# Performance work log

Measured on AMD Instinct MI355X. Metric: run time of the kernel, lower is better.

Reference implementation:

```python
import jax, jax.numpy as jnp
import numpy as np

# cfg constants (init_kwargs)
NMS_THRESH = 0.6
CONF_THRESH = 0.05
TOPN = 1000           # nms_thresh_topN: pre-NMS cap and post-NMS cap
NUM_CLASSES = 80
CLS_OFFSET = 4096.0   # > max image coord; class-aware NMS via coordinate offset


def setup_inputs() -> dict:
    key = jax.random.key(0)
    k0, k1, k2, k3 = jax.random.split(key, 4)
    B, H, W, C = 16, 128, 128, NUM_CLASSES
    N = H * W
    image_h, image_w = 1024, 1024
    # anchor-point pixel coordinates for this FPN level
    locations = jax.random.uniform(k0, (N, 2), dtype=jnp.float32) * 1024.0
    pred_cls = jax.random.normal(k1, (B, H, W, C), dtype=jnp.float32)
    # (l, t, r, b) distances are positive
    pred_boxes = jax.random.uniform(k2, (B, H, W, 4), dtype=jnp.float32) * 64.0
    pred_centerness = jax.random.normal(k3, (B, H, W), dtype=jnp.float32)
    return {"locations": locations, "pred_cls": pred_cls, "pred_boxes": pred_boxes,
            "pred_centerness": pred_centerness, "image_h": image_h, "image_w": image_w}


def _pairwise_iou(b):  # b: [K, 4] xyxy
    x1, y1, x2, y2 = b[:, 0], b[:, 1], b[:, 2], b[:, 3]
    area = jnp.maximum(x2 - x1, 0.0) * jnp.maximum(y2 - y1, 0.0)
    ix1 = jnp.maximum(x1[:, None], x1[None, :])
    iy1 = jnp.maximum(y1[:, None], y1[None, :])
    ix2 = jnp.minimum(x2[:, None], x2[None, :])
    iy2 = jnp.minimum(y2[:, None], y2[None, :])
    inter = jnp.maximum(ix2 - ix1, 0.0) * jnp.maximum(iy2 - iy1, 0.0)
    return inter / (area[:, None] + area[None, :] - inter + 1e-9)


def _nms_keep(iou, valid):
    # greedy NMS over score-descending candidates; iou: [B,K,K], valid: [B,K] bool
    K = iou.shape[-1]
    ar = jnp.arange(K)

    def body(i, keep):
        iou_i = jax.lax.dynamic_index_in_dim(iou, i, axis=1, keepdims=False)  # [B,K]
        keep_i = jnp.take(keep, i, axis=1)                                    # [B]
        sup = (iou_i > NMS_THRESH) & (ar[None, :] > i) & keep_i[:, None]
        return keep & ~sup

    return jax.lax.fori_loop(0, K, body, valid)


def reference(locations, pred_cls, pred_boxes, pred_centerness, image_h, image_w):
    B, H, W, C = pred_cls.shape
    N = H * W
    cls = jax.nn.sigmoid(pred_cls.reshape(B, N, C))
    ctr = jax.nn.sigmoid(pred_centerness.reshape(B, N))
    boxes = pred_boxes.reshape(B, N, 4)
    scores = cls * ctr[:, :, None]                    # [B,N,C]
    mask = cls > CONF_THRESH
    neg = jnp.asarray(-jnp.inf, scores.dtype)
    flat = jnp.where(mask, scores, neg).reshape(B, N * C)
    # pre-NMS top-K over masked (location, class) candidates; emulates
    # cls_mask_top_n = clamp(mask.sum(), max=topN) + topk in the torch code
    vals, idx = jax.lax.top_k(flat, TOPN)             # [B,K]
    valid = jnp.isfinite(vals)
    loc_i = idx // C                                  # location index
    lab = idx % C + 1                                 # 1-based class label
    pb = jnp.take_along_axis(boxes, loc_i[:, :, None], axis=1)   # [B,K,4] (l,t,r,b)
    locs = locations[loc_i]                                       # [B,K,2]
    x1 = jnp.clip(locs[..., 0] - pb[..., 0], 0.0, image_w - 1)
    y1 = jnp.clip(locs[..., 1] - pb[..., 1], 0.0, image_h - 1)
    x2 = jnp.clip(locs[..., 0] + pb[..., 2], 0.0, image_w - 1)
    y2 = jnp.clip(locs[..., 1] + pb[..., 3], 0.0, image_h - 1)
    det = jnp.stack([x1, y1, x2, y2], axis=-1)        # [B,K,4] xyxy, clipped
    score = jnp.where(valid, vals, 0.0)
    # sort by score descending for greedy NMS
    order = jnp.argsort(-score, axis=1)
    score = jnp.take_along_axis(score, order, axis=1)
    valid = jnp.take_along_axis(valid, order, axis=1)
    lab = jnp.take_along_axis(lab, order, axis=1)
    det = jnp.take_along_axis(det, order[:, :, None], axis=1)
    # per-class NMS via class-offset trick (boxes of different classes never overlap)
    iou = jax.vmap(_pairwise_iou)(det + lab.astype(det.dtype)[:, :, None] * CLS_OFFSET)
    keep = _nms_keep(iou, valid) & valid
    # final topN (nms_thresh_topN) is a no-op here: candidates <= TOPN already
    boxes_out = det * keep[:, :, None].astype(det.dtype)
    scores_out = jnp.where(keep, score, 0.0)
    labels_out = jnp.where(keep, lab, 0)
    return boxes_out, scores_out, labels_out
```

## Files before the change

### kernel.cpp

```cpp
#include <hip/hip_runtime.h>

#define B_    16
#define N_    16384
#define C_    80
#define NC_   (N_ * C_)
#define TOPN_ 1000
#define T0_   0.70f
#define T0KEY_ 0x3F333333u
#define RKEY_  0x3E800000u
#define NBIN_  512
#define BSH_   15
#define BLKCAP_ 128
#define RESCCAP_ 8192

#define OFF_CNT    0u
#define OFF_CAND   16384u
#define OFF_RESC   (16384u + 4194304u)

__device__ __forceinline__ float sigm(float x) { return 1.0f / (1.0f + expf(-x)); }

__device__ __forceinline__ int binof(unsigned key) {
    int b = (int)((key - RKEY_) >> BSH_);
    return b > (NBIN_ - 1) ? (NBIN_ - 1) : b;
}
__device__ __forceinline__ unsigned key_lb(int b) {
    return RKEY_ + ((unsigned)b << BSH_);
}

__global__ __launch_bounds__(256, 4) void k_pass1(const float* __restrict__ cls,
                                                  const float* __restrict__ ctr,
                                                  unsigned* __restrict__ cnt,
                                                  unsigned long long* __restrict__ cand) {
    __shared__ float xh[64];
    __shared__ float sbv[64];
    __shared__ unsigned long long stage[BLKCAP_];
    __shared__ unsigned lcnt;
    const int blk = blockIdx.x, t = threadIdx.x;
    const int b = blk >> 8, k = blk & 255;
    if (t == 0) lcnt = 0;
    if (t < 64) {
        float sc = sigm(ctr[b * N_ + k * 64 + t]);
        sbv[t] = sc;
        float q = T0_ / sc;
        xh[t] = (q < 1.f) ? (logf(q / (1.f - q)) - 1e-3f) : 3.0e38f;
    }
    __syncthreads();
    const float4* p = (const float4*)(cls + (size_t)b * NC_ + (size_t)k * 5120);
    float4 v[5];
    #pragma unroll
    for (int i = 0; i < 5; ++i) v[i] = p[5 * t + i];
    const int r = t >> 2;
    const float thr = xh[r];
    float mx = v[0].x;
    #pragma unroll
    for (int i = 0; i < 5; ++i)
        mx = fmaxf(mx, fmaxf(fmaxf(v[i].x, v[i].y), fmaxf(v[i].z, v[i].w)));
    if (mx >= thr) {
        const float sb = sbv[r];
        #pragma unroll
        for (int i = 0; i < 5; ++i) {
            float xs[4] = {v[i].x, v[i].y, v[i].z, v[i].w};
            #pragma unroll
            for (int j = 0; j < 4; ++j) {
                if (xs[j] >= thr) {
                    float sapx = sb * __builtin_amdgcn_rcpf(1.f + __expf(-xs[j]));
                    if (sapx >= T0_ * 0.999f) {
                        float s = sigm(xs[j]);
                        unsigned key = __float_as_uint(s * sb);
                        if (key >= T0KEY_) {
                            unsigned pos = atomicAdd(&lcnt, 1u);
                            if (pos < (unsigned)BLKCAP_) {
                                unsigned e = (unsigned)(k * 5120 + (5 * t + i) * 4 + j);
                                stage[pos] = ((unsigned long long)key << 32) |
                                             (unsigned long long)(0xFFFFFFFFu - e);
                            }
                        }
                    }
                }
            }
        }
    }
    __syncthreads();
    unsigned lc = lcnt; if (lc > (unsigned)BLKCAP_) lc = (unsigned)BLKCAP_;
    if (t == 0) cnt[blk] = lc;
    unsigned long long* seg = cand + ((size_t)blk << 7);
    for (unsigned i = t; i < lc; i += 256) seg[i] = stage[i];
}

union TailSMem {
    struct {
        unsigned hbin[NBIN_];
        unsigned binBase[NBIN_];
        unsigned long long srt[2048];
        unsigned long long srt2[1024];
    } s;
    struct {
        float4 bxo[1024];
        unsigned short clsList[1024];
        unsigned clsStart[81];
        unsigned clsCur[81];
        unsigned short supIdx[1024 * 16];
        unsigned char nsup[1024];
    } c;
};

__global__ __launch_bounds__(1024) void k_tail(
        const unsigned long long* __restrict__ cand, const unsigned* __restrict__ cnt,
        unsigned long long* __restrict__ resc,
        const float* __restrict__ boxes, const float* __restrict__ locs,
        const int* __restrict__ ph, const int* __restrict__ pw,
        const float* __restrict__ cls, const float* __restrict__ ctr,
        float* __restrict__ out) {
    __shared__ TailSMem u;
    __shared__ unsigned csh[256];
    __shared__ unsigned Lsh, totSh, rcnt, rcwSh;
    __shared__ unsigned long long keepw[16];
    __shared__ unsigned long long vmaskSh[16];
    const int b = blockIdx.x, t = threadIdx.x;

    if (t == 0) { rcnt = 0; rcwSh = 0; }
    if (t < 256) {
        unsigned cc = cnt[b * 256 + t];
        csh[t] = cc > (unsigned)BLKCAP_ ? (unsigned)BLKCAP_ : cc;
    }
    __syncthreads();
    if (t < 64) {
        unsigned s4 = csh[4 * t] + csh[4 * t + 1] + csh[4 * t + 2] + csh[4 * t + 3];
        #pragma unroll
        for (int off = 32; off >= 1; off >>= 1) s4 += __shfl_down(s4, off, 64);
        if (t == 0) totSh = s4;
    }
    __syncthreads();
    if (totSh < (unsigned)TOPN_) {
        unsigned long long* rsw = resc + ((size_t)b << 13);
        const float4* p = (const float4*)(cls + (size_t)b * NC_);
        for (unsigned f = t; f < (unsigned)(NC_ / 4); f += 1024) {
            float4 v = p[f];
            unsigned nl = f / 20;
            float sb = sigm(ctr[b * N_ + nl]);
            float xs[4] = {v.x, v.y, v.z, v.w};
            #pragma unroll
            for (int j = 0; j < 4; ++j) {
                float s = sigm(xs[j]);
                if (s > 0.05f) {
                    unsigned key = __float_as_uint(s * sb);
                    if (key >= RKEY_ && key < T0KEY_) {
                        unsigned pos = atomicAdd(&rcnt, 1u);
                        if (pos < (unsigned)RESCCAP_) {
                            unsigned e = 4u * f + (unsigned)j;
                            rsw[pos] = ((unsigned long long)key << 32) |
                                       (unsigned long long)(0xFFFFFFFFu - e);
                        }
                    }
                }
            }
        }
        __syncthreads();
        if (t == 0) {
            unsigned rc = rcnt;
            rcwSh = rc > (unsigned)RESCCAP_ ? (unsigned)RESCCAP_ : rc;
        }
        __syncthreads();
    }

    if (t < NBIN_) u.s.hbin[t] = 0;
    u.s.srt[t] = 0ull; u.s.srt[t + 1024] = 0ull;
    u.s.srt2[t] = 0ull;
    __syncthreads();
    const unsigned long long* g = cand + ((size_t)b << 15);
    const unsigned long long* rs = resc + ((size_t)b << 13);
    const unsigned rcw = rcwSh;
    {
        const int s = t >> 2;
        const unsigned cc = csh[s];
        const unsigned long long* gs = g + ((size_t)s << 7);
        for (unsigned o = 2u * (unsigned)(t & 3); o < cc; o += 8) {
            unsigned long long c0 = gs[o];
            unsigned long long c1 = (o + 1 < cc) ? gs[o + 1] : 0ull;
            atomicAdd(&u.s.hbin[binof((unsigned)(c0 >> 32))], 1u);
            if (o + 1 < cc)
                atomicAdd(&u.s.hbin[binof((unsigned)(c1 >> 32))], 1u);
        }
    }
    for (unsigned o = t; o < rcw; o += 1024)
        atomicAdd(&u.s.hbin[binof((unsigned)(rs[o] >> 32))], 1u);
    __syncthreads();
    if (t < 64) {
        const int l = t;
        unsigned cs = 0;
        #pragma unroll
        for (int i = 0; i < 8; ++i) cs += u.s.hbin[8 * l + i];
        unsigned S = cs;
        #pragma unroll
        for (int off = 1; off < 64; off <<= 1) {
            unsigned y = __shfl_down(S, off, 64);
            if (l + off < 64) S += y;
        }
        unsigned acc = S - cs;
        int bc_l = NBIN_;
        #pragma unroll
        for (int b2 = 7; b2 >= 0; --b2) {
            int bin = 8 * l + b2;
            u.s.binBase[bin] = acc;
            if (acc < (unsigned)TOPN_) bc_l = bin;
            acc += u.s.hbin[bin];
        }
        #pragma unroll
        for (int off = 1; off < 64; off <<= 1) {
            int y = __shfl_down(bc_l, off, 64);
            bc_l = bc_l < y ? bc_l : y;
        }
        if (l == 0) Lsh = key_lb(bc_l < NBIN_ ? bc_l : 0);
    }
    __syncthreads();
    const unsigned Lk = Lsh;
    {
        const int s = t >> 2;
        const unsigned cc = csh[s];
        const unsigned long long* gs = g + ((size_t)s << 7);
        for (unsigned o = 2u * (unsigned)(t & 3); o < cc; o += 8) {
            unsigned long long c0 = gs[o];
            unsigned long long c1 = (o + 1 < cc) ? gs[o + 1] : 0ull;
            unsigned k0 = (unsigned)(c0 >> 32);
            if (k0 >= Lk) {
                unsigned slot = atomicAdd(&u.s.binBase[binof(k0)], 1u);
                if (slot < 2048u) u.s.srt[slot] = c0;
            }
            if (o + 1 < cc) {
                unsigned k1 = (unsigned)(c1 >> 32);
                if (k1 >= Lk) {
                    unsigned slot = atomicAdd(&u.s.binBase[binof(k1)], 1u);
                    if (slot < 2048u) u.s.srt[slot] = c1;
                }
            }
        }
    }
    for (unsigned o = t; o < rcw; o += 1024) {
        unsigned long long comp = rs[o];
        unsigned key = (unsigned)(comp >> 32);
        if (key >= Lk) {
            unsigned slot = atomicAdd(&u.s.binBase[binof(key)], 1u);
            if (slot < 2048u) u.s.srt[slot] = comp;
        }
    }
    __syncthreads();
    #pragma unroll
    for (int pp = 0; pp < 2; ++pp) {
        unsigned p = (unsigned)t + 1024u * pp;
        unsigned long long comp = u.s.srt[p];
        if (comp) {
            int bin = binof((unsigned)(comp >> 32));
            unsigned endq = u.s.binBase[bin];
            unsigned pop = u.s.hbin[bin];
            unsigned beg = endq - pop;
            unsigned end2 = endq > 2048u ? 2048u : endq;
            unsigned rank = 0;
            for (unsigned j = beg; j < end2; ++j) rank += (u.s.srt[j] > comp);
            unsigned pos = beg + rank;
            if (pos < 1024u) u.s.srt2[pos] = comp;
        }
    }
    __syncthreads();
    unsigned long long comp = u.s.srt2[t];
    unsigned key = (unsigned)(comp >> 32);
    float4 d = {0.f, 0.f, 0.f, 0.f}, doff = {0.f, 0.f, 0.f, 0.f};
    float sc = 0.f; int lb = 0;
    if (key) {
        unsigned idx = 0xFFFFFFFFu - (unsigned)comp;
        unsigned loc = idx / (unsigned)C_;
        unsigned cc2 = idx - loc * (unsigned)C_;
        lb = (int)cc2 + 1;
        float4 pb = ((const float4*)boxes)[(size_t)b * N_ + loc];
        float lx = locs[2 * loc], ly = locs[2 * loc + 1];
        float Wm1 = (float)(pw[0] - 1), Hm1 = (float)(ph[0] - 1);
        d.x = fminf(fmaxf(lx - pb.x, 0.f), Wm1);
        d.y = fminf(fmaxf(ly - pb.y, 0.f), Hm1);
        d.z = fminf(fmaxf(lx + pb.z, 0.f), Wm1);
        d.w = fminf(fmaxf(ly + pb.w, 0.f), Hm1);
        sc = __uint_as_float(key);
        float off = (float)lb * 4096.0f;
        doff.x = d.x + off; doff.y = d.y + off; doff.z = d.z + off; doff.w = d.w + off;
    }
    const bool valid = (key != 0u);
    {
        unsigned long long ball = __ballot(valid);
        if ((t & 63) == 0) vmaskSh[t >> 6] = ball;
    }
    __syncthreads();

    u.c.bxo[t] = doff;
    if (t < 81) u.c.clsStart[t] = 0;
    __syncthreads();
    if (lb > 0) atomicAdd(&u.c.clsStart[lb], 1u);
    __syncthreads();
    if (t < 64) {
        const int l = t;
        unsigned s0 = 0, s1 = 0;
        if (l < 40) { s0 = u.c.clsStart[2 * l + 1]; s1 = u.c.clsStart[2 * l + 2]; }
        unsigned p = s0 + s1;
        unsigned S = p;
        #pragma unroll
        for (int off = 1; off < 64; off <<= 1) {
            unsigned y = __shfl_up(S, off, 64);
            if (l >= off) S += y;
        }
        unsigned excl = S - p;
        if (l < 40) {
            u.c.clsStart[2 * l + 1] = excl;
            u.c.clsCur[2 * l + 1]   = excl;
            u.c.clsStart[2 * l + 2] = excl + s0;
            u.c.clsCur[2 * l + 2]   = excl + s0;
        }
    }
    __syncthreads();
    if (lb > 0) {
        unsigned pos = atomicAdd(&u.c.clsCur[lb], 1u);
        u.c.clsList[pos] = (unsigned short)t;
    }
    __syncthreads();
    unsigned nsup = 0;
    if (valid) {
        float4 A = doff;
        float aA = fmaxf(A.z - A.x, 0.f) * fmaxf(A.w - A.y, 0.f);
        unsigned beg = u.c.clsStart[lb], end = u.c.clsCur[lb];
        for (unsigned q = beg; q < end; ++q) {
            int j = (int)u.c.clsList[q];
            if (j < t) {
                float4 Bv = u.c.bxo[j];
                float aB = fmaxf(Bv.z - Bv.x, 0.f) * fmaxf(Bv.w - Bv.y, 0.f);
                float ix1 = fmaxf(A.x, Bv.x), iy1 = fmaxf(A.y, Bv.y);
                float ix2 = fminf(A.z, Bv.z), iy2 = fminf(A.w, Bv.w);
                float inter = fmaxf(ix2 - ix1, 0.f) * fmaxf(iy2 - iy1, 0.f);
                float iou = inter / (aA + aB - inter + 1e-9f);
                if (iou > 0.6f) {
                    if (nsup < 16u) u.c.supIdx[t * 16 + nsup] = (unsigned short)j;
                    ++nsup;
                }
            }
        }
        if (nsup > 16u) nsup = 16u;
    }
    u.c.nsup[t] = (unsigned char)nsup;
    __syncthreads();

    if (t < 64) {
        const int ii = t;
        for (int gg = 0; gg < 16; ++gg) {
            const int row = gg * 64 + ii;
            const unsigned base = (unsigned)(gg << 6);
            unsigned ns = u.c.nsup[row];
            unsigned long long diag = 0;
            bool supP = false;
            for (unsigned q = 0; q < ns; ++q) {
                unsigned j = (unsigned)u.c.supIdx[row * 16 + q];
                if (j < base) {
                    if ((keepw[j >> 6] >> (j & 63)) & 1ull) supP = true;
                } else {
                    diag |= 1ull << (j & 63);
                }
            }
            bool alive = (((vmaskSh[gg] >> ii) & 1ull) != 0) && !supP;
            unsigned long long undec = __ballot(alive);
            unsigned long long kept = 0;
            while (undec) {
                bool meU = ((undec >> ii) & 1ull) != 0;
                bool supK = (kept & diag) != 0;
                bool anyU = (undec & diag) != 0;
                unsigned long long bkm = __ballot(meU && !supK && !anyU);
                unsigned long long brm = __ballot(meU && supK);
                kept |= bkm;
                undec &= ~(bkm | brm);
            }
            if (ii == 0) keepw[gg] = kept;
        }
    }
    __syncthreads();

    if (t < TOPN_) {
        bool kp = ((keepw[t >> 6] >> (t & 63)) & 1ull) != 0;
        ((float4*)out)[(size_t)b * TOPN_ + t] = kp ? d : make_float4(0.f, 0.f, 0.f, 0.f);
        out[B_ * TOPN_ * 4 + b * TOPN_ + t] = kp ? sc : 0.f;
        out[B_ * TOPN_ * 5 + b * TOPN_ + t] = kp ? (float)lb : 0.f;
    }
}

extern "C" void kernel_launch(void* const* d_in, const int* in_sizes, int n_in,
                              void* d_out, int out_size, void* d_ws, size_t ws_size,
                              hipStream_t stream) {
    (void)in_sizes; (void)n_in; (void)out_size; (void)ws_size;
    const float* locations = (const float*)d_in[0];
    const float* pred_cls  = (const float*)d_in[1];
    const float* pred_box  = (const float*)d_in[2];
    const float* pred_ctr  = (const float*)d_in[3];
    const int*   ph        = (const int*)d_in[4];
    const int*   pw        = (const int*)d_in[5];
    float* out = (float*)d_out;

    char* w = (char*)d_ws;
    unsigned* cnt            = (unsigned*)(w + OFF_CNT);
    unsigned long long* cand = (unsigned long long*)(w + OFF_CAND);
    unsigned long long* resc = (unsigned long long*)(w + OFF_RESC);


    k_pass1<<<4096, 256, 0, stream>>>(pred_cls, pred_ctr, cnt, cand);
    k_tail<<<B_, 1024, 0, stream>>>(cand, cnt, resc, pred_box, locations, ph, pw,
                                    pred_cls, pred_ctr, out);
}
```

Measured before the change: 166.5 us.

## Fuse candidate pass and NMS tail into one cooperative kernel with grid sync

Combines the candidate-filter pass and the per-batch tail into a single cooperative launch of 256 blocks of 1024 threads, separated by a grid-wide sync. Each block now handles a 1024-row segment instead of 64 rows, so there are 16 segments per batch with larger staging buffers. The aim is to remove the second kernel launch and its gap. The trade-off is fewer, larger blocks in the streaming phase, which may reduce memory-level parallelism, plus a grid barrier during which 240 blocks sit idle. If the cooperative launch fails, the code falls back to two separate launches.

```diff
diff --git a/kernel.cpp b/kernel.cpp
--- a/kernel.cpp
+++ b/kernel.cpp
@@ -1,4 +1,6 @@
 #include <hip/hip_runtime.h>
+#include <hip/hip_cooperative_groups.h>
+namespace cg = cooperative_groups;
 
 #define B_    16
 #define N_    16384
@@ -10,12 +12,13 @@
 #define RKEY_  0x3E800000u
 #define NBIN_  512
 #define BSH_   15
-#define BLKCAP_ 128
+#define NSEG_  16
+#define SEGCAP_ 2048
 #define RESCCAP_ 8192
 
 #define OFF_CNT    0u
-#define OFF_CAND   16384u
-#define OFF_RESC   (16384u + 4194304u)
+#define OFF_CAND   1024u
+#define OFF_RESC   (1024u + 4194304u)
 
 __device__ __forceinline__ float sigm(float x) { return 1.0f / (1.0f + expf(-x)); }
 
@@ -27,52 +30,58 @@
     return RKEY_ + ((unsigned)b << BSH_);
 }
 
-__global__ __launch_bounds__(256, 4) void k_pass1(const float* __restrict__ cls,
-                                                  const float* __restrict__ ctr,
-                                                  unsigned* __restrict__ cnt,
-                                                  unsigned long long* __restrict__ cand) {
-    __shared__ float xh[64];
-    __shared__ float sbv[64];
-    __shared__ unsigned long long stage[BLKCAP_];
+__device__ __forceinline__ void phaseP(const float* __restrict__ cls,
+                                       const float* __restrict__ ctr,
+                                       unsigned* __restrict__ cnt,
+                                       unsigned long long* __restrict__ cand,
+                                       int bb, int t) {
+    __shared__ float xh[1024];
+    __shared__ float sbv[1024];
+    __shared__ unsigned long long stage[SEGCAP_];
     __shared__ unsigned lcnt;
-    const int blk = blockIdx.x, t = threadIdx.x;
-    const int b = blk >> 8, k = blk & 255;
+    const int b = bb >> 4, seg = bb & 15;
     if (t == 0) lcnt = 0;
-    if (t < 64) {
-        float sc = sigm(ctr[b * N_ + k * 64 + t]);
-        sbv[t] = sc;
-        float q = T0_ / sc;
+    {
+        int row = seg * 1024 + t;
+        float scv = sigm(ctr[b * N_ + row]);
+        sbv[t] = scv;
+        float q = T0_ / scv;
         xh[t] = (q < 1.f) ? (logf(q / (1.f - q)) - 1e-3f) : 3.0e38f;
     }
     __syncthreads();
-    const float4* p = (const float4*)(cls + (size_t)b * NC_ + (size_t)k * 5120);
-    float4 v[5];
-    #pragma unroll
-    for (int i = 0; i < 5; ++i) v[i] = p[5 * t + i];
-    const int r = t >> 2;
-    const float thr = xh[r];
-    float mx = v[0].x;
-    #pragma unroll
-    for (int i = 0; i < 5; ++i)
-        mx = fmaxf(mx, fmaxf(fmaxf(v[i].x, v[i].y), fmaxf(v[i].z, v[i].w)));
-    if (mx >= thr) {
-        const float sb = sbv[r];
-        #pragma unroll
-        for (int i = 0; i < 5; ++i) {
-            float xs[4] = {v[i].x, v[i].y, v[i].z, v[i].w};
+    const int r256 = t >> 2;
+    for (int it = 0; it < 4; ++it) {
+        const int lrow = it * 256 + r256;
+        const float4* p = (const float4*)(cls + (size_t)b * NC_ +
+                            ((size_t)seg * 1024 + (size_t)it * 256) * C_);
+        float4 v[5];
+        #pragma unroll
+        for (int i = 0; i < 5; ++i) v[i] = p[5 * t + i];
+        const float thr = xh[lrow];
+        float mx = v[0].x;
+        #pragma unroll
+        for (int i = 0; i < 5; ++i)
+            mx = fmaxf(mx, fmaxf(fmaxf(v[i].x, v[i].y), fmaxf(v[i].z, v[i].w)));
+        if (mx >= thr) {
+            const float sb = sbv[lrow];
             #pragma unroll
-            for (int j = 0; j < 4; ++j) {
-                if (xs[j] >= thr) {
-                    float sapx = sb * __builtin_amdgcn_rcpf(1.f + __expf(-xs[j]));
-                    if (sapx >= T0_ * 0.999f) {
-                        float s = sigm(xs[j]);
-                        unsigned key = __float_as_uint(s * sb);
-                        if (key >= T0KEY_) {
-                            unsigned pos = atomicAdd(&lcnt, 1u);
-                            if (pos < (unsigned)BLKCAP_) {
-                                unsigned e = (unsigned)(k * 5120 + (5 * t + i) * 4 + j);
-                                stage[pos] = ((unsigned long long)key << 32) |
-                                             (unsigned long long)(0xFFFFFFFFu - e);
+            for (int i = 0; i < 5; ++i) {
+                float xs[4] = {v[i].x, v[i].y, v[i].z, v[i].w};
+                #pragma unroll
+                for (int j = 0; j < 4; ++j) {
+                    if (xs[j] >= thr) {
+                        float sapx = sb * __builtin_amdgcn_rcpf(1.f + __expf(-xs[j]));
+                        if (sapx >= T0_ * 0.999f) {
+                            float s = sigm(xs[j]);
+                            unsigned key = __float_as_uint(s * sb);
+                            if (key >= T0KEY_) {
+                                unsigned pos = atomicAdd(&lcnt, 1u);
+                                if (pos < (unsigned)SEGCAP_) {
+                                    unsigned e = (unsigned)((seg * 1024 + lrow) * 80 +
+                                                 (t & 3) * 20 + i * 4 + j);
+                                    stage[pos] = ((unsigned long long)key << 32) |
+                                                 (unsigned long long)(0xFFFFFFFFu - e);
+                                }
                             }
                         }
                     }
@@ -81,13 +90,13 @@
         }
     }
     __syncthreads();
-    unsigned lc = lcnt; if (lc > (unsigned)BLKCAP_) lc = (unsigned)BLKCAP_;
-    if (t == 0) cnt[blk] = lc;
-    unsigned long long* seg = cand + ((size_t)blk << 7);
-    for (unsigned i = t; i < lc; i += 256) seg[i] = stage[i];
-}
-
-union TailSMem {
+    unsigned lc = lcnt; if (lc > (unsigned)SEGCAP_) lc = (unsigned)SEGCAP_;
+    if (t == 0) cnt[bb] = lc;
+    unsigned long long* segp = cand + ((size_t)bb << 11);
+    for (unsigned i = t; i < lc; i += 1024) segp[i] = stage[i];
+}
+
+union TailU {
     struct {
         unsigned hbin[NBIN_];
         unsigned binBase[NBIN_];
@@ -104,40 +113,42 @@
     } c;
 };
 
-__global__ __launch_bounds__(1024) void k_tail(
-        const unsigned long long* __restrict__ cand, const unsigned* __restrict__ cnt,
-        unsigned long long* __restrict__ resc,
-        const float* __restrict__ boxes, const float* __restrict__ locs,
-        const int* __restrict__ ph, const int* __restrict__ pw,
-        const float* __restrict__ cls, const float* __restrict__ ctr,
-        float* __restrict__ out) {
-    __shared__ TailSMem u;
-    __shared__ unsigned csh[256];
+__device__ __forceinline__ void tailF(const unsigned long long* __restrict__ cand,
+                                      const unsigned* __restrict__ cnt,
+                                      unsigned long long* __restrict__ resc,
+                                      const float* __restrict__ boxes,
+                                      const float* __restrict__ locs,
+                                      const int* __restrict__ ph,
+                                      const int* __restrict__ pw,
+                                      const float* __restrict__ cls,
+                                      const float* __restrict__ ctr,
+                                      float* __restrict__ out, int batch, int t) {
+    __shared__ TailU u;
+    __shared__ unsigned csh[NSEG_];
     __shared__ unsigned Lsh, totSh, rcnt, rcwSh;
     __shared__ unsigned long long keepw[16];
     __shared__ unsigned long long vmaskSh[16];
-    const int b = blockIdx.x, t = threadIdx.x;
 
     if (t == 0) { rcnt = 0; rcwSh = 0; }
-    if (t < 256) {
-        unsigned cc = cnt[b * 256 + t];
-        csh[t] = cc > (unsigned)BLKCAP_ ? (unsigned)BLKCAP_ : cc;
+    if (t < NSEG_) {
+        unsigned cc = cnt[batch * NSEG_ + t];
+        csh[t] = cc > (unsigned)SEGCAP_ ? (unsigned)SEGCAP_ : cc;
     }
     __syncthreads();
     if (t < 64) {
-        unsigned s4 = csh[4 * t] + csh[4 * t + 1] + csh[4 * t + 2] + csh[4 * t + 3];
+        unsigned s4 = (t < NSEG_) ? csh[t] : 0u;
         #pragma unroll
         for (int off = 32; off >= 1; off >>= 1) s4 += __shfl_down(s4, off, 64);
         if (t == 0) totSh = s4;
     }
     __syncthreads();
     if (totSh < (unsigned)TOPN_) {
-        unsigned long long* rsw = resc + ((size_t)b << 13);
-        const float4* p = (const float4*)(cls + (size_t)b * NC_);
+        unsigned long long* rsw = resc + ((size_t)batch << 13);
+        const float4* p = (const float4*)(cls + (size_t)batch * NC_);
         for (unsigned f = t; f < (unsigned)(NC_ / 4); f += 1024) {
             float4 v = p[f];
             unsigned nl = f / 20;
-            float sb = sigm(ctr[b * N_ + nl]);
+            float sb = sigm(ctr[batch * N_ + nl]);
             float xs[4] = {v.x, v.y, v.z, v.w};
             #pragma unroll
             for (int j = 0; j < 4; ++j) {
@@ -167,14 +178,14 @@
     u.s.srt[t] = 0ull; u.s.srt[t + 1024] = 0ull;
     u.s.srt2[t] = 0ull;
     __syncthreads();
-    const unsigned long long* g = cand + ((size_t)b << 15);
-    const unsigned long long* rs = resc + ((size_t)b << 13);
+    const unsigned long long* g = cand + ((size_t)batch << 15);
+    const unsigned long long* rs = resc + ((size_t)batch << 13);
     const unsigned rcw = rcwSh;
     {
-        const int s = t >> 2;
+        const int s = t >> 6;
         const unsigned cc = csh[s];
-        const unsigned long long* gs = g + ((size_t)s << 7);
-        for (unsigned o = 2u * (unsigned)(t & 3); o < cc; o += 8) {
+        const unsigned long long* gs = g + ((size_t)s << 11);
+        for (unsigned o = 2u * (unsigned)(t & 63); o < cc; o += 128) {
             unsigned long long c0 = gs[o];
             unsigned long long c1 = (o + 1 < cc) ? gs[o + 1] : 0ull;
             atomicAdd(&u.s.hbin[binof((unsigned)(c0 >> 32))], 1u);
@@ -215,10 +226,10 @@
     __syncthreads();
     const unsigned Lk = Lsh;
     {
-        const int s = t >> 2;
+        const int s = t >> 6;
         const unsigned cc = csh[s];
-        const unsigned long long* gs = g + ((size_t)s << 7);
-        for (unsigned o = 2u * (unsigned)(t & 3); o < cc; o += 8) {
+        const unsigned long long* gs = g + ((size_t)s << 11);
+        for (unsigned o = 2u * (unsigned)(t & 63); o < cc; o += 128) {
             unsigned long long c0 = gs[o];
             unsigned long long c1 = (o + 1 < cc) ? gs[o + 1] : 0ull;
             unsigned k0 = (unsigned)(c0 >> 32);
@@ -270,7 +281,7 @@
         unsigned loc = idx / (unsigned)C_;
         unsigned cc2 = idx - loc * (unsigned)C_;
         lb = (int)cc2 + 1;
-        float4 pb = ((const float4*)boxes)[(size_t)b * N_ + loc];
+        float4 pb = ((const float4*)boxes)[(size_t)batch * N_ + loc];
         float lx = locs[2 * loc], ly = locs[2 * loc + 1];
         float Wm1 = (float)(pw[0] - 1), Hm1 = (float)(ph[0] - 1);
         d.x = fminf(fmaxf(lx - pb.x, 0.f), Wm1);
@@ -378,10 +389,39 @@
 
     if (t < TOPN_) {
         bool kp = ((keepw[t >> 6] >> (t & 63)) & 1ull) != 0;
-        ((float4*)out)[(size_t)b * TOPN_ + t] = kp ? d : make_float4(0.f, 0.f, 0.f, 0.f);
-        out[B_ * TOPN_ * 4 + b * TOPN_ + t] = kp ? sc : 0.f;
-        out[B_ * TOPN_ * 5 + b * TOPN_ + t] = kp ? (float)lb : 0.f;
-    }
+        ((float4*)out)[(size_t)batch * TOPN_ + t] = kp ? d : make_float4(0.f, 0.f, 0.f, 0.f);
+        out[B_ * TOPN_ * 4 + batch * TOPN_ + t] = kp ? sc : 0.f;
+        out[B_ * TOPN_ * 5 + batch * TOPN_ + t] = kp ? (float)lb : 0.f;
+    }
+}
+
+__global__ __launch_bounds__(1024) void k_all(
+        const float* __restrict__ cls, const float* __restrict__ ctr,
+        const float* __restrict__ boxes, const float* __restrict__ locs,
+        const int* __restrict__ ph, const int* __restrict__ pw,
+        unsigned* __restrict__ cnt, unsigned long long* __restrict__ cand,
+        unsigned long long* __restrict__ resc, float* __restrict__ out) {
+    const int bb = blockIdx.x, t = threadIdx.x;
+    phaseP(cls, ctr, cnt, cand, bb, t);
+    cg::this_grid().sync();
+    if (bb < B_)
+        tailF(cand, cnt, resc, boxes, locs, ph, pw, cls, ctr, out, bb, t);
+}
+
+__global__ __launch_bounds__(1024) void k_pass(
+        const float* __restrict__ cls, const float* __restrict__ ctr,
+        unsigned* __restrict__ cnt, unsigned long long* __restrict__ cand) {
+    phaseP(cls, ctr, cnt, cand, blockIdx.x, threadIdx.x);
+}
+__global__ __launch_bounds__(1024) void k_tailk(
+        const unsigned long long* __restrict__ cand, const unsigned* __restrict__ cnt,
+        unsigned long long* __restrict__ resc,
+        const float* __restrict__ boxes, const float* __restrict__ locs,
+        const int* __restrict__ ph, const int* __restrict__ pw,
+        const float* __restrict__ cls, const float* __restrict__ ctr,
+        float* __restrict__ out) {
+    tailF(cand, cnt, resc, boxes, locs, ph, pw, cls, ctr, out,
+          blockIdx.x, threadIdx.x);
 }
 
 extern "C" void kernel_launch(void* const* d_in, const int* in_sizes, int n_in,
@@ -401,8 +441,14 @@
     unsigned long long* cand = (unsigned long long*)(w + OFF_CAND);
     unsigned long long* resc = (unsigned long long*)(w + OFF_RESC);
 
-
-    k_pass1<<<4096, 256, 0, stream>>>(pred_cls, pred_ctr, cnt, cand);
-    k_tail<<<B_, 1024, 0, stream>>>(cand, cnt, resc, pred_box, locations, ph, pw,
-                                    pred_cls, pred_ctr, out);
-}
+    void* args[] = {(void*)&pred_cls, (void*)&pred_ctr, (void*)&pred_box,
+                    (void*)&locations, (void*)&ph, (void*)&pw,
+                    (void*)&cnt, (void*)&cand, (void*)&resc, (void*)&out};
+    hipError_t err = hipLaunchCooperativeKernel((const void*)k_all, dim3(256),
+                                                dim3(1024), args, 0, stream);
+    if (err != hipSuccess) {
+        k_pass<<<256, 1024, 0, stream>>>(pred_cls, pred_ctr, cnt, cand);
+        k_tailk<<<B_, 1024, 0, stream>>>(cand, cnt, resc, pred_box, locations,
+                                         ph, pw, pred_cls, pred_ctr, out);
+    }
+}
```

New measurement: 202.4 us. 21.5% more time.
